# Performance work log

Hardware: AMD Instinct MI355X
Metric: run time of the kernel (lower is better)

Reference implementation:

```python
import jax, jax.numpy as jnp
import numpy as np

L = 1000  # fixed waveform length implied by MaxPool1d(1000) and [:, :, :1000] slices


def _conv1d(x, w, pad, reflect=False):
    # x: [B, Cin, T], w: [Cout, Cin, K]; torch conv1d == cross-correlation == lax conv
    if reflect:
        x = jnp.pad(x, ((0, 0), (0, 0), (pad, pad)), mode='reflect')
        pads = [(0, 0)]
    else:
        pads = [(pad, pad)]
    return jax.lax.conv_general_dilated(x, w, (1,), pads,
                                        dimension_numbers=('NCH', 'OIH', 'NCH'))


def setup_inputs() -> dict:
    key = jax.random.key(0)
    ks = jax.random.split(key, 10)
    B = 4096
    s = 0.1  # weight init scale
    return {
        'wf': jax.random.normal(ks[0], (B, 1, L), jnp.float32),
        'mask': jnp.ones((B, L), jnp.float32),
        'SPE': jax.random.uniform(ks[1], (L,), jnp.float32),
        'w_cum_area': jax.random.normal(ks[2], (1, 1, 121), jnp.float32) * s,
        'w_x': jax.random.normal(ks[3], (1, 1, 121), jnp.float32) * s,
        'w_div': jax.random.normal(ks[4], (1, 1, 121), jnp.float32) * s,
        'w_roll': jax.random.normal(ks[5], (1, 1, 101), jnp.float32) * s,
        'w_sub': jax.random.normal(ks[6], (15, 3, 21), jnp.float32) * s,
        'w_comb': jax.random.normal(ks[7], (1, 1, 5, 101, 3), jnp.float32) * s,
        'W_param': jnp.array([0.0, 5.0, 10.0], jnp.float32),
    }


def reference(wf, mask, SPE, w_cum_area, w_x, w_div, w_roll, w_sub, w_comb, W_param):
    B = wf.shape[0]
    # fixed (non-learned) derivative + running-mean kernels from __init__
    div_x_w = jnp.array([1/280, -4/105, 1/5, -4/5, 0.0, 4/5, -1/5, 4/105, -1/280],
                        jnp.float32).reshape(1, 1, 9)
    run_mean_w = jnp.full((1, 1, 51), 1.0 / 51, jnp.float32)

    # h = MaxPool1d(1000)(wf).squeeze(1).tile(1,3) / SPE.amax(); tiling == broadcast
    h = wf.max(axis=(1, 2))[:, None] / SPE.max()            # [B,1]
    W = jax.nn.softmax(-jax.nn.relu(h - W_param), axis=1)   # [B,3]

    cum_area = jnp.cumsum(wf, axis=-1)                      # [B,1,L]
    div_x_smd = _conv1d(_conv1d(wf, div_x_w, 4), run_mean_w, 25)  # zero-padded convs

    BL = _conv1d(cum_area, w_roll, 100, reflect=True)[:, :, :L] * w_cum_area.sum()
    fit_cum = jax.nn.relu(_conv1d(cum_area, w_cum_area, 100, reflect=True)[:, :, :L] - BL)
    fit_x = jax.nn.relu(_conv1d(wf, w_x, 100, reflect=True))[:, :, :L]
    fit_div = jax.nn.relu(_conv1d(div_x_smd, w_div, 100, reflect=True))[:, :, :L]

    features1 = jnp.concatenate([fit_cum, fit_x, fit_div], axis=1)   # [B,3,L]
    S = features1.sum(axis=2, keepdims=True) + 1e-10
    features1_norm = features1 / S

    features2 = _conv1d(features1_norm, w_sub, 10, reflect=True)     # [B,15,L]
    # [B,L,15] -> [B,L,5,3], weight the 3-way split by per-sample W
    fc = features2.transpose(0, 2, 1).reshape(B, L, 5, 3) * W[:, None, None, :]
    fc = fc.transpose(0, 2, 1, 3)[:, None]                           # [B,1,5,L,3]

    out = jax.lax.conv_general_dilated(fc, w_comb, (1, 1, 1),
                                       [(0, 0), (50, 50), (0, 0)],
                                       dimension_numbers=('NCDHW', 'OIDHW', 'NCDHW'))
    out = jax.nn.softplus(out).reshape(B, L)                         # [B,L]

    amax = out.max(axis=1, keepdims=True) + 1e-10
    out_norm = out / amax * mask
    return jax.nn.softmax(1e4 * out_norm, axis=1)
```

## Files before the change

kernel.cpp:

```cpp
#include <hip/hip_runtime.h>
#include <math.h>

#define TPB 256
#define LW  1000
#define CSTR 1124

#define OFF_WFE   0
#define OFF_CUME  1200
#define OFF_DSE   2400
#define OFF_F1E   3600
#define OFF_D1    3600
#define OFF_SCAND 4600
#define OFF_OUTB  6972
#define OFF_RED   7972
#define SMEM_F    7980
#define OFF_KC    0
#define OFF_WS2   384
#define OFF_F2V   1344

__device__ __forceinline__ float4 ld4(const float* p) { return *(const float4*)p; }

__device__ __forceinline__ float blk_red_max(float v, float* red) {
  #pragma unroll
  for (int o = 32; o > 0; o >>= 1) v = fmaxf(v, __shfl_xor(v, o, 64));
  const int w = threadIdx.x >> 6;
  if ((threadIdx.x & 63) == 0) red[w] = v;
  __syncthreads();
  float r = fmaxf(fmaxf(red[0], red[1]), fmaxf(red[2], red[3]));
  __syncthreads();
  return r;
}

__device__ __forceinline__ float blk_red_sum(float v, float* red) {
  #pragma unroll
  for (int o = 32; o > 0; o >>= 1) v += __shfl_xor(v, o, 64);
  const int w = threadIdx.x >> 6;
  if ((threadIdx.x & 63) == 0) red[w] = v;
  __syncthreads();
  float r = red[0] + red[1] + red[2] + red[3];
  __syncthreads();
  return r;
}

__device__ __forceinline__ int refl(int j) {
  return j < 0 ? -j : (j >= LW ? 2 * LW - 2 - j : j);
}

extern "C" __global__ void prep_kernel(const float* __restrict__ wsub_g,
                                       const float* __restrict__ wcb_g,
                                       float* __restrict__ P) {
  const int task = blockIdx.x * blockDim.x + threadIdx.x;
  if (task >= 1089) return;
  const int m = task / 363;
  const int r = task - m * 363;
  const int cin = r / 121;
  const int k = r - cin * 121;
  float acc = 0.f;
  for (int q = 0; q < 5; ++q) {
    const int ch = 3 * q + m;
    const float* ws = wsub_g + (ch * 3 + cin) * 21;
    #pragma unroll
    for (int j = 0; j < 21; ++j) {
      const int a = k - j;
      if (a >= 0 && a <= 100) acc = fmaf(ws[j], wcb_g[q * 303 + a * 3 + m], acc);
    }
  }
  P[task] = acc;
}

extern "C" __global__ void __launch_bounds__(TPB, 5)
spot_kernel(const float* __restrict__ wf_g,  const float* __restrict__ mask_g,
            const float* __restrict__ spe_g, const float* __restrict__ wca_g,
            const float* __restrict__ wx_g,  const float* __restrict__ wdv_g,
            const float* __restrict__ wrl_g, const float* __restrict__ wsub_g,
            const float* __restrict__ wcb_g, const float* __restrict__ wp_g,
            const float* __restrict__ P_g,   float* __restrict__ out_g)
{
  __shared__ __align__(16) float sm[SMEM_F];
  const int tid = threadIdx.x;
  const int b = blockIdx.x;
  const float* wf = wf_g + (size_t)b * LW;
  float* red = sm + OFF_RED;

  float hmx = -INFINITY;
  for (int i = tid; i < 1200; i += TPB) sm[OFF_WFE + i] = wf[refl(i - 100)];
  for (int t = tid; t < LW; t += TPB) hmx = fmaxf(hmx, wf[t]);
  float smx = -INFINITY;
  for (int t = tid; t < LW; t += TPB) smx = fmaxf(smx, spe_g[t]);
  double* scand = (double*)(sm + OFF_SCAND);
  double l0 = 0, l1 = 0, l2 = 0, l3 = 0;
  if (tid < 250) {
    l0 = (double)wf[4 * tid + 0];
    l1 = l0 + (double)wf[4 * tid + 1];
    l2 = l1 + (double)wf[4 * tid + 2];
    l3 = l2 + (double)wf[4 * tid + 3];
  }
  scand[tid] = l3;

  hmx = blk_red_max(hmx, red);
  smx = blk_red_max(smx, red);

  const float h = hmx / smx;
  float a0 = -fmaxf(h - wp_g[0], 0.f);
  float a1 = -fmaxf(h - wp_g[1], 0.f);
  float a2 = -fmaxf(h - wp_g[2], 0.f);
  float am = fmaxf(a0, fmaxf(a1, a2));
  float e0 = expf(a0 - am), e1 = expf(a1 - am), e2 = expf(a2 - am);
  float es = e0 + e1 + e2;
  float Wv[3] = { e0 / es, e1 / es, e2 / es };
  float swca = 0.f;
  for (int k = 0; k < 121; ++k) swca += wca_g[k];

  if (tid < 64) {
    double s0 = scand[4 * tid], s1 = scand[4 * tid + 1];
    double s2 = scand[4 * tid + 2], s3 = scand[4 * tid + 3];
    double tot = s0 + s1 + s2 + s3;
    double inc = tot;
    #pragma unroll
    for (int o = 1; o < 64; o <<= 1) {
      double n = __shfl_up(inc, o, 64);
      if ((tid & 63) >= o) inc += n;
    }
    double ex = inc - tot;
    scand[4 * tid]     = ex;
    scand[4 * tid + 1] = ex + s0;
    scand[4 * tid + 2] = ex + s0 + s1;
    scand[4 * tid + 3] = ex + s0 + s1 + s2;
  }
  __syncthreads();
  if (tid < 250) {
    double base = scand[tid];
    float4 cv = { (float)(base + l0), (float)(base + l1),
                  (float)(base + l2), (float)(base + l3) };
    *(float4*)(sm + OFF_CUME + 100 + 4 * tid) = cv;
  }
  const float dker[9] = {1.f/280.f, -4.f/105.f, 0.2f, -0.8f, 0.f, 0.8f, -0.2f, 4.f/105.f, -1.f/280.f};
  for (int t = tid; t < LW; t += TPB) {
    float a = 0.f;
    #pragma unroll
    for (int k = 0; k < 9; ++k) {
      if (k == 4) continue;
      int j = t + k - 4;
      float x = (j >= 0 && j < LW) ? sm[OFF_WFE + 100 + j] : 0.f;
      a = fmaf(dker[k], x, a);
    }
    sm[OFF_D1 + t] = a;
  }
  __syncthreads();
  for (int i = tid; i < 100; i += TPB) {
    sm[OFF_CUME + i]        = sm[OFF_CUME + 200 - i];
    sm[OFF_CUME + 1100 + i] = sm[OFF_CUME + 1098 - i];
  }
  for (int t = tid; t < LW; t += TPB) {
    int lo = t - 25 < 0 ? 0 : t - 25;
    int hi = t + 25 >= LW ? LW - 1 : t + 25;
    float a = 0.f;
    for (int j = lo; j <= hi; ++j) a += sm[OFF_D1 + j];
    sm[OFF_DSE + 100 + t] = a * (1.f / 51.f);
  }
  __syncthreads();
  for (int i = tid; i < 100; i += TPB) {
    sm[OFF_DSE + i]        = sm[OFF_DSE + 200 - i];
    sm[OFF_DSE + 1100 + i] = sm[OFF_DSE + 1098 - i];
  }
  __syncthreads();

  float lsC = 0.f, lsX = 0.f, lsD = 0.f;
  if (tid < 250) {
    const int t0 = 4 * tid;
    const float* ce = sm + OFF_CUME + t0;
    const float* we = sm + OFF_WFE + t0;
    const float* de = sm + OFF_DSE + t0;
    float cw_[8], ww_[8], dw_[8];
    *(float4*)cw_ = ld4(ce); *(float4*)(cw_ + 4) = ld4(ce + 4);
    *(float4*)ww_ = ld4(we); *(float4*)(ww_ + 4) = ld4(we + 4);
    *(float4*)dw_ = ld4(de); *(float4*)(dw_ + 4) = ld4(de + 4);
    float aC[4] = {0,0,0,0}, aB[4] = {0,0,0,0}, aX[4] = {0,0,0,0}, aD[4] = {0,0,0,0};
    for (int g = 0; g < 120; g += 4) {
      #pragma unroll
      for (int kk = 0; kk < 4; ++kk) {
        const int k = g + kk;
        const float wa = wca_g[k], wxk = wx_g[k], wdk = wdv_g[k];
        #pragma unroll
        for (int j = 0; j < 4; ++j) {
          aC[j] = fmaf(wa,  cw_[kk + j], aC[j]);
          aX[j] = fmaf(wxk, ww_[kk + j], aX[j]);
          aD[j] = fmaf(wdk, dw_[kk + j], aD[j]);
        }
        if (k <= 100) {
          const float wr = wrl_g[k];
          #pragma unroll
          for (int j = 0; j < 4; ++j) aB[j] = fmaf(wr, cw_[kk + j], aB[j]);
        }
      }
      #pragma unroll
      for (int j = 0; j < 4; ++j) { cw_[j] = cw_[j+4]; ww_[j] = ww_[j+4]; dw_[j] = dw_[j+4]; }
      *(float4*)(cw_ + 4) = ld4(ce + g + 8);
      *(float4*)(ww_ + 4) = ld4(we + g + 8);
      *(float4*)(dw_ + 4) = ld4(de + g + 8);
    }
    {
      const float wa = wca_g[120], wxk = wx_g[120], wdk = wdv_g[120];
      #pragma unroll
      for (int j = 0; j < 4; ++j) {
        aC[j] = fmaf(wa,  cw_[j], aC[j]);
        aX[j] = fmaf(wxk, ww_[j], aX[j]);
        aD[j] = fmaf(wdk, dw_[j], aD[j]);
      }
    }
    float4 vC, vX, vD;
    float* pC = (float*)&vC; float* pX = (float*)&vX; float* pD = (float*)&vD;
    #pragma unroll
    for (int j = 0; j < 4; ++j) {
      float fc = fmaxf(fmaf(-aB[j], swca, aC[j]), 0.f);
      float fx = fmaxf(aX[j], 0.f);
      float fd = fmaxf(aD[j], 0.f);
      pC[j] = fc; pX[j] = fx; pD[j] = fd;
      lsC += fc; lsX += fx; lsD += fd;
    }
    *(float4*)(sm + OFF_F1E + 0 * CSTR + 60 + t0) = vC;
    *(float4*)(sm + OFF_F1E + 1 * CSTR + 60 + t0) = vX;
    *(float4*)(sm + OFF_F1E + 2 * CSTR + 60 + t0) = vD;
  }
  const float SC = blk_red_sum(lsC, red) + 1e-10f;
  const float SX = blk_red_sum(lsX, red) + 1e-10f;
  const float SD = blk_red_sum(lsD, red) + 1e-10f;
  {
    const float iC = 1.f / SC, iX = 1.f / SX, iD = 1.f / SD;
    for (int t = tid; t < LW; t += TPB) {
      sm[OFF_F1E + 0 * CSTR + 60 + t] *= iC;
      sm[OFF_F1E + 1 * CSTR + 60 + t] *= iX;
      sm[OFF_F1E + 2 * CSTR + 60 + t] *= iD;
    }
  }
  __syncthreads();

  for (int i = tid; i < 372; i += TPB) {
    const int c = i / 124, j = i - c * 124;
    const int dst = (j < 60) ? j : (1000 + j);
    const int src = (j < 60) ? (120 - j) : (1118 - j);
    sm[OFF_F1E + c * CSTR + dst] = sm[OFF_F1E + c * CSTR + src];
  }
  for (int i = tid; i < 363; i += TPB) {
    const int cin = i / 121, k = i - cin * 121;
    const float* Pp = P_g + cin * 121 + k;
    sm[OFF_KC + cin * 124 + k] =
        fmaf(Wv[0], Pp[0], fmaf(Wv[1], Pp[363], Wv[2] * Pp[726]));
  }
  for (int i = tid; i < 945; i += TPB) sm[OFF_WS2 + i] = wsub_g[i];
  __syncthreads();

  if (tid < 250) {
    const int t0 = 4 * tid;
    float acc[4] = {0,0,0,0};
    #pragma unroll
    for (int cin = 0; cin < 3; ++cin) {
      const float* xr = sm + OFF_F1E + cin * CSTR + t0;
      const float* kc = sm + OFF_KC + cin * 124;
      float xw[8];
      *(float4*)xw = ld4(xr); *(float4*)(xw + 4) = ld4(xr + 4);
      for (int g = 0; g < 120; g += 4) {
        #pragma unroll
        for (int kk = 0; kk < 4; ++kk) {
          const float w = kc[g + kk];
          #pragma unroll
          for (int j = 0; j < 4; ++j) acc[j] = fmaf(w, xw[kk + j], acc[j]);
        }
        #pragma unroll
        for (int j = 0; j < 4; ++j) xw[j] = xw[j + 4];
        *(float4*)(xw + 4) = ld4(xr + g + 8);
      }
      const float w120 = kc[120];
      #pragma unroll
      for (int j = 0; j < 4; ++j) acc[j] = fmaf(w120, xw[j], acc[j]);
    }
    float4 st = {acc[0], acc[1], acc[2], acc[3]};
    *(float4*)(sm + OFF_OUTB + t0) = st;
  }
  for (int task = tid; task < 1500; task += TPB) {
    const int ch = task / 100, up = task - ch * 100;
    const int u = (up < 50) ? (up - 50) : (950 + up);
    float acc2 = 0.f;
    #pragma unroll
    for (int cin = 0; cin < 3; ++cin) {
      const float* xr = sm + OFF_F1E + cin * CSTR + (50 + u);
      const float* wr = sm + OFF_WS2 + (ch * 3 + cin) * 21;
      #pragma unroll
      for (int j = 0; j < 21; ++j) acc2 = fmaf(wr[j], xr[j], acc2);
    }
    sm[OFF_F2V + ch * 100 + up] = acc2;
  }
  __syncthreads();

  if (tid < 100) {
    float corr = 0.f;
    if (tid < 50) {
      const int t = tid;
      for (int a = 0; a < 50; ++a) {
        if (t + a <= 49) {
          const int up = t + a;
          #pragma unroll
          for (int m = 0; m < 3; ++m) {
            const float wvm = Wv[m];
            #pragma unroll
            for (int q = 0; q < 5; ++q)
              corr = fmaf(wvm * wcb_g[q * 303 + a * 3 + m],
                          sm[OFF_F2V + (3 * q + m) * 100 + up], corr);
          }
        }
      }
      sm[OFF_OUTB + t] -= corr;
    } else {
      const int tp = tid;
      const int t = 900 + tp;
      for (int d = 0; d < 50; ++d) {
        if (tp - d >= 50) {
          const int up = tp - d;
          const int a = 100 - d;
          #pragma unroll
          for (int m = 0; m < 3; ++m) {
            const float wvm = Wv[m];
            #pragma unroll
            for (int q = 0; q < 5; ++q)
              corr = fmaf(wvm * wcb_g[q * 303 + a * 3 + m],
                          sm[OFF_F2V + (3 * q + m) * 100 + up], corr);
          }
        }
      }
      sm[OFF_OUTB + t] -= corr;
    }
  }
  __syncthreads();

  float lm = -INFINITY;
  for (int t = tid; t < LW; t += TPB) {
    float z = sm[OFF_OUTB + t];
    float sp = fmaxf(z, 0.f) + log1pf(expf(-fabsf(z)));
    sm[OFF_OUTB + t] = sp;
    lm = fmaxf(lm, sp);
  }
  const float amax = blk_red_max(lm, red) + 1e-10f;
  const float* mrow = mask_g + (size_t)b * LW;
  float lm2 = -INFINITY;
  for (int t = tid; t < LW; t += TPB) {
    float v = 1e4f * (sm[OFF_OUTB + t] / amax) * mrow[t];
    sm[OFF_OUTB + t] = v;
    lm2 = fmaxf(lm2, v);
  }
  const float m2 = blk_red_max(lm2, red);
  float ls = 0.f;
  for (int t = tid; t < LW; t += TPB) {
    float e = expf(sm[OFF_OUTB + t] - m2);
    sm[OFF_OUTB + t] = e;
    ls += e;
  }
  const float S2 = blk_red_sum(ls, red);
  const float invs = 1.f / S2;
  float* orow = out_g + (size_t)b * LW;
  for (int t = tid; t < LW; t += TPB) orow[t] = sm[OFF_OUTB + t] * invs;
}

extern "C" void kernel_launch(void* const* d_in, const int* in_sizes, int n_in,
                              void* d_out, int out_size, void* d_ws, size_t ws_size,
                              hipStream_t stream) {
  (void)n_in; (void)ws_size; (void)out_size;
  const float* wf   = (const float*)d_in[0];
  const float* mask = (const float*)d_in[1];
  const float* spe  = (const float*)d_in[2];
  const float* wca  = (const float*)d_in[3];
  const float* wx   = (const float*)d_in[4];
  const float* wdv  = (const float*)d_in[5];
  const float* wrl  = (const float*)d_in[6];
  const float* wsub = (const float*)d_in[7];
  const float* wcb  = (const float*)d_in[8];
  const float* wp   = (const float*)d_in[9];
  float* P = (float*)d_ws;
  const int B = in_sizes[0] / LW;
  hipLaunchKernelGGL(prep_kernel, dim3(5), dim3(TPB), 0, stream, wsub, wcb, P);
  hipLaunchKernelGGL(spot_kernel, dim3(B), dim3(TPB), 0, stream,
                     wf, mask, spe, wca, wx, wdv, wrl, wsub, wcb, wp, P, (float*)d_out);
}
```

Baseline: 338.2 us.

## Use prefix-sum running mean, hoist SPE max and weight sum, keep outputs in registers

The 51-tap running mean is now computed as a difference of a prefix sum of the derivative signal. The SPE max and the w_cum_area sum move into the prep kernel, and the wf loads are vectorised. The edge-correction convolution is restructured into vectorised blocked tasks. The final softplus/softmax stages keep each thread's four outputs in registers instead of a shared buffer, which shrinks shared memory and allows raising launch bounds from 5 to 6 blocks. A float prefix sum may lose some precision compared with the direct 51-term sum.

```diff
diff --git a/kernel.cpp b/kernel.cpp
--- a/kernel.cpp
+++ b/kernel.cpp
@@ -6,17 +6,17 @@
 #define CSTR 1124
 
 #define OFF_WFE   0
-#define OFF_CUME  1200
-#define OFF_DSE   2400
-#define OFF_F1E   3600
-#define OFF_D1    3600
-#define OFF_SCAND 4600
-#define OFF_OUTB  6972
-#define OFF_RED   7972
-#define SMEM_F    7980
+#define OFF_CUME  1120
+#define OFF_DSE   2240
+#define OFF_F1E   3360
+#define OFF_SCAND 3360
+#define OFF_C     3872
+#define OFF_RED   6740
+#define SMEM_F    6748
 #define OFF_KC    0
-#define OFF_WS2   384
-#define OFF_F2V   1344
+#define OFF_WS2   376
+#define OFF_F2V   1456
+#define OFF_PART  0
 
 __device__ __forceinline__ float4 ld4(const float* p) { return *(const float4*)p; }
 
@@ -46,29 +46,71 @@
   return j < 0 ? -j : (j >= LW ? 2 * LW - 2 - j : j);
 }
 
+template<int OFF0>
+__device__ __forceinline__ void f2v_accum(const float* xr, const float* wr, float acc[4]) {
+  float xw[12];
+  *(float4*)xw       = ld4(xr);
+  *(float4*)(xw + 4) = ld4(xr + 4);
+  *(float4*)(xw + 8) = ld4(xr + 8);
+  #pragma unroll
+  for (int jb = 0; jb < 20; jb += 4) {
+    float4 w4 = ld4(wr + jb);
+    const float wv[4] = {w4.x, w4.y, w4.z, w4.w};
+    #pragma unroll
+    for (int kk = 0; kk < 4; ++kk)
+      #pragma unroll
+      for (int o = 0; o < 4; ++o)
+        acc[o] = fmaf(wv[kk], xw[OFF0 + kk + o], acc[o]);
+    #pragma unroll
+    for (int j = 0; j < 8; ++j) xw[j] = xw[j + 4];
+    *(float4*)(xw + 8) = ld4(xr + jb + 12);
+  }
+  const float w20 = wr[20];
+  #pragma unroll
+  for (int o = 0; o < 4; ++o) acc[o] = fmaf(w20, xw[OFF0 + o], acc[o]);
+}
+
 extern "C" __global__ void prep_kernel(const float* __restrict__ wsub_g,
                                        const float* __restrict__ wcb_g,
+                                       const float* __restrict__ wca_g,
+                                       const float* __restrict__ spe_g,
                                        float* __restrict__ P) {
+  __shared__ float sred[4];
   const int task = blockIdx.x * blockDim.x + threadIdx.x;
-  if (task >= 1089) return;
-  const int m = task / 363;
-  const int r = task - m * 363;
-  const int cin = r / 121;
-  const int k = r - cin * 121;
-  float acc = 0.f;
-  for (int q = 0; q < 5; ++q) {
-    const int ch = 3 * q + m;
-    const float* ws = wsub_g + (ch * 3 + cin) * 21;
-    #pragma unroll
-    for (int j = 0; j < 21; ++j) {
-      const int a = k - j;
-      if (a >= 0 && a <= 100) acc = fmaf(ws[j], wcb_g[q * 303 + a * 3 + m], acc);
-    }
-  }
-  P[task] = acc;
-}
-
-extern "C" __global__ void __launch_bounds__(TPB, 5)
+  if (task < 1089) {
+    const int m = task / 363;
+    const int r = task - m * 363;
+    const int cin = r / 121;
+    const int k = r - cin * 121;
+    float acc = 0.f;
+    for (int q = 0; q < 5; ++q) {
+      const int ch = 3 * q + m;
+      const float* ws = wsub_g + (ch * 3 + cin) * 21;
+      #pragma unroll
+      for (int j = 0; j < 21; ++j) {
+        const int a = k - j;
+        if (a >= 0 && a <= 100) acc = fmaf(ws[j], wcb_g[q * 303 + a * 3 + m], acc);
+      }
+    }
+    P[task] = acc;
+  } else if (task == 1089) {
+    float s = 0.f;
+    for (int k = 0; k < 121; ++k) s += wca_g[k];
+    P[1089] = s;
+  }
+  if (blockIdx.x == 4) {
+    float mx = -INFINITY;
+    for (int t = threadIdx.x; t < LW; t += TPB) mx = fmaxf(mx, spe_g[t]);
+    #pragma unroll
+    for (int o = 32; o > 0; o >>= 1) mx = fmaxf(mx, __shfl_xor(mx, o, 64));
+    if ((threadIdx.x & 63) == 0) sred[threadIdx.x >> 6] = mx;
+    __syncthreads();
+    if (threadIdx.x == 0)
+      P[1090] = fmaxf(fmaxf(sred[0], sred[1]), fmaxf(sred[2], sred[3]));
+  }
+}
+
+extern "C" __global__ void __launch_bounds__(TPB, 6)
 spot_kernel(const float* __restrict__ wf_g,  const float* __restrict__ mask_g,
             const float* __restrict__ spe_g, const float* __restrict__ wca_g,
             const float* __restrict__ wx_g,  const float* __restrict__ wdv_g,
@@ -81,25 +123,25 @@
   const int b = blockIdx.x;
   const float* wf = wf_g + (size_t)b * LW;
   float* red = sm + OFF_RED;
-
-  float hmx = -INFINITY;
-  for (int i = tid; i < 1200; i += TPB) sm[OFF_WFE + i] = wf[refl(i - 100)];
-  for (int t = tid; t < LW; t += TPB) hmx = fmaxf(hmx, wf[t]);
-  float smx = -INFINITY;
-  for (int t = tid; t < LW; t += TPB) smx = fmaxf(smx, spe_g[t]);
+  const int t0 = 4 * tid;
+
+  for (int i = tid; i < 1120; i += TPB) sm[OFF_WFE + i] = wf[refl(i - 100)];
   double* scand = (double*)(sm + OFF_SCAND);
   double l0 = 0, l1 = 0, l2 = 0, l3 = 0;
-  if (tid < 250) {
-    l0 = (double)wf[4 * tid + 0];
-    l1 = l0 + (double)wf[4 * tid + 1];
-    l2 = l1 + (double)wf[4 * tid + 2];
-    l3 = l2 + (double)wf[4 * tid + 3];
+  float hmx = -INFINITY;
+  if (tid < 250) {
+    float4 wv4 = ld4(wf + t0);
+    hmx = fmaxf(fmaxf(wv4.x, wv4.y), fmaxf(wv4.z, wv4.w));
+    l0 = (double)wv4.x;
+    l1 = l0 + (double)wv4.y;
+    l2 = l1 + (double)wv4.z;
+    l3 = l2 + (double)wv4.w;
   }
   scand[tid] = l3;
-
   hmx = blk_red_max(hmx, red);
-  smx = blk_red_max(smx, red);
-
+
+  const float smx = P_g[1090];
+  const float swca = P_g[1089];
   const float h = hmx / smx;
   float a0 = -fmaxf(h - wp_g[0], 0.f);
   float a1 = -fmaxf(h - wp_g[1], 0.f);
@@ -108,8 +150,6 @@
   float e0 = expf(a0 - am), e1 = expf(a1 - am), e2 = expf(a2 - am);
   float es = e0 + e1 + e2;
   float Wv[3] = { e0 / es, e1 / es, e2 / es };
-  float swca = 0.f;
-  for (int k = 0; k < 121; ++k) swca += wca_g[k];
 
   if (tid < 64) {
     double s0 = scand[4 * tid], s1 = scand[4 * tid + 1];
@@ -132,42 +172,79 @@
     double base = scand[tid];
     float4 cv = { (float)(base + l0), (float)(base + l1),
                   (float)(base + l2), (float)(base + l3) };
-    *(float4*)(sm + OFF_CUME + 100 + 4 * tid) = cv;
+    *(float4*)(sm + OFF_CUME + 100 + t0) = cv;
   }
   const float dker[9] = {1.f/280.f, -4.f/105.f, 0.2f, -0.8f, 0.f, 0.8f, -0.2f, 4.f/105.f, -1.f/280.f};
+  float dv0 = 0, dv1 = 0, dv2 = 0, dv3 = 0;
+  if (tid >= 1 && tid <= 248) {
+    float xw[12];
+    const float* xr = sm + OFF_WFE + t0 + 96;
+    *(float4*)xw = ld4(xr); *(float4*)(xw+4) = ld4(xr+4); *(float4*)(xw+8) = ld4(xr+8);
+    float d[4];
+    #pragma unroll
+    for (int j = 0; j < 4; ++j) {
+      float a = 0.f;
+      #pragma unroll
+      for (int k = 0; k < 9; ++k) {
+        if (k == 4) continue;
+        a = fmaf(dker[k], xw[j + k], a);
+      }
+      d[j] = a;
+    }
+    dv0 = d[0]; dv1 = d[1]; dv2 = d[2]; dv3 = d[3];
+  } else if (tid == 0 || tid == 249) {
+    float d[4];
+    #pragma unroll
+    for (int j = 0; j < 4; ++j) {
+      float a = 0.f;
+      for (int k = 0; k < 9; ++k) {
+        if (k == 4) continue;
+        const int o = t0 + j - 4 + k;
+        if (o >= 0 && o < LW) a = fmaf(dker[k], sm[OFF_WFE + 100 + o], a);
+      }
+      d[j] = a;
+    }
+    dv0 = d[0]; dv1 = d[1]; dv2 = d[2]; dv3 = d[3];
+  }
+  {
+    const float s0 = dv0, s1 = s0 + dv1, s2 = s1 + dv2, s3 = s2 + dv3;
+    float inc = s3;
+    const int lane = tid & 63;
+    #pragma unroll
+    for (int o = 1; o < 64; o <<= 1) {
+      float n = __shfl_up(inc, o, 64);
+      if (lane >= o) inc += n;
+    }
+    float* redw = red + 4;
+    if (lane == 63) redw[tid >> 6] = inc;
+    __syncthreads();
+    float base = 0.f;
+    for (int w = 0; w < (tid >> 6); ++w) base += redw[w];
+    if (tid < 250) {
+      const float ex = base + inc - s3;
+      float4 cv = { ex + s0, ex + s1, ex + s2, ex + s3 };
+      *(float4*)(sm + OFF_C + t0) = cv;
+    }
+  }
+  __syncthreads();
   for (int t = tid; t < LW; t += TPB) {
-    float a = 0.f;
-    #pragma unroll
-    for (int k = 0; k < 9; ++k) {
-      if (k == 4) continue;
-      int j = t + k - 4;
-      float x = (j >= 0 && j < LW) ? sm[OFF_WFE + 100 + j] : 0.f;
-      a = fmaf(dker[k], x, a);
-    }
-    sm[OFF_D1 + t] = a;
-  }
-  __syncthreads();
-  for (int i = tid; i < 100; i += TPB) {
-    sm[OFF_CUME + i]        = sm[OFF_CUME + 200 - i];
-    sm[OFF_CUME + 1100 + i] = sm[OFF_CUME + 1098 - i];
-  }
-  for (int t = tid; t < LW; t += TPB) {
-    int lo = t - 25 < 0 ? 0 : t - 25;
-    int hi = t + 25 >= LW ? LW - 1 : t + 25;
-    float a = 0.f;
-    for (int j = lo; j <= hi; ++j) a += sm[OFF_D1 + j];
-    sm[OFF_DSE + 100 + t] = a * (1.f / 51.f);
-  }
-  __syncthreads();
-  for (int i = tid; i < 100; i += TPB) {
-    sm[OFF_DSE + i]        = sm[OFF_DSE + 200 - i];
-    sm[OFF_DSE + 1100 + i] = sm[OFF_DSE + 1098 - i];
+    const float hi = sm[OFF_C + (t + 25 > 999 ? 999 : t + 25)];
+    const float lo = (t >= 26) ? sm[OFF_C + t - 26] : 0.f;
+    sm[OFF_DSE + 100 + t] = (hi - lo) * (1.f / 51.f);
+  }
+  for (int i = tid; i < 120; i += TPB) {
+    if (i < 100) sm[OFF_CUME + i] = sm[OFF_CUME + 200 - i];
+    else         sm[OFF_CUME + 1000 + i] = sm[OFF_CUME + 2198 - (1000 + i)];
+  }
+  __syncthreads();
+  for (int i = tid; i < 120; i += TPB) {
+    if (i < 100) sm[OFF_DSE + i] = sm[OFF_DSE + 200 - i];
+    else         sm[OFF_DSE + 1000 + i] = sm[OFF_DSE + 2198 - (1000 + i)];
   }
   __syncthreads();
 
   float lsC = 0.f, lsX = 0.f, lsD = 0.f;
   if (tid < 250) {
-    const int t0 = 4 * tid;
     const float* ce = sm + OFF_CUME + t0;
     const float* we = sm + OFF_WFE + t0;
     const float* de = sm + OFF_DSE + t0;
@@ -176,7 +253,31 @@
     *(float4*)ww_ = ld4(we); *(float4*)(ww_ + 4) = ld4(we + 4);
     *(float4*)dw_ = ld4(de); *(float4*)(dw_ + 4) = ld4(de + 4);
     float aC[4] = {0,0,0,0}, aB[4] = {0,0,0,0}, aX[4] = {0,0,0,0}, aD[4] = {0,0,0,0};
-    for (int g = 0; g < 120; g += 4) {
+    for (int g = 0; g < 100; g += 4) {
+      #pragma unroll
+      for (int kk = 0; kk < 4; ++kk) {
+        const int k = g + kk;
+        const float wa = wca_g[k], wxk = wx_g[k], wdk = wdv_g[k], wr = wrl_g[k];
+        #pragma unroll
+        for (int j = 0; j < 4; ++j) {
+          aC[j] = fmaf(wa,  cw_[kk + j], aC[j]);
+          aB[j] = fmaf(wr,  cw_[kk + j], aB[j]);
+          aX[j] = fmaf(wxk, ww_[kk + j], aX[j]);
+          aD[j] = fmaf(wdk, dw_[kk + j], aD[j]);
+        }
+      }
+      #pragma unroll
+      for (int j = 0; j < 4; ++j) { cw_[j] = cw_[j+4]; ww_[j] = ww_[j+4]; dw_[j] = dw_[j+4]; }
+      *(float4*)(cw_ + 4) = ld4(ce + g + 8);
+      *(float4*)(ww_ + 4) = ld4(we + g + 8);
+      *(float4*)(dw_ + 4) = ld4(de + g + 8);
+    }
+    {
+      const float wr100 = wrl_g[100];
+      #pragma unroll
+      for (int j = 0; j < 4; ++j) aB[j] = fmaf(wr100, cw_[j], aB[j]);
+    }
+    for (int g = 100; g < 116; g += 4) {
       #pragma unroll
       for (int kk = 0; kk < 4; ++kk) {
         const int k = g + kk;
@@ -187,11 +288,6 @@
           aX[j] = fmaf(wxk, ww_[kk + j], aX[j]);
           aD[j] = fmaf(wdk, dw_[kk + j], aD[j]);
         }
-        if (k <= 100) {
-          const float wr = wrl_g[k];
-          #pragma unroll
-          for (int j = 0; j < 4; ++j) aB[j] = fmaf(wr, cw_[kk + j], aB[j]);
-        }
       }
       #pragma unroll
       for (int j = 0; j < 4; ++j) { cw_[j] = cw_[j+4]; ww_[j] = ww_[j+4]; dw_[j] = dw_[j+4]; }
@@ -199,13 +295,15 @@
       *(float4*)(ww_ + 4) = ld4(we + g + 8);
       *(float4*)(dw_ + 4) = ld4(de + g + 8);
     }
-    {
-      const float wa = wca_g[120], wxk = wx_g[120], wdk = wdv_g[120];
+    #pragma unroll
+    for (int kk = 0; kk < 5; ++kk) {
+      const int k = 116 + kk;
+      const float wa = wca_g[k], wxk = wx_g[k], wdk = wdv_g[k];
       #pragma unroll
       for (int j = 0; j < 4; ++j) {
-        aC[j] = fmaf(wa,  cw_[j], aC[j]);
-        aX[j] = fmaf(wxk, ww_[j], aX[j]);
-        aD[j] = fmaf(wdk, dw_[j], aD[j]);
+        aC[j] = fmaf(wa,  cw_[kk + j], aC[j]);
+        aX[j] = fmaf(wxk, ww_[kk + j], aX[j]);
+        aD[j] = fmaf(wdk, dw_[kk + j], aD[j]);
       }
     }
     float4 vC, vX, vD;
@@ -235,8 +333,8 @@
   }
   __syncthreads();
 
-  for (int i = tid; i < 372; i += TPB) {
-    const int c = i / 124, j = i - c * 124;
+  for (int i = tid; i < 360; i += TPB) {
+    const int c = i / 120, j = i - c * 120;
     const int dst = (j < 60) ? j : (1000 + j);
     const int src = (j < 60) ? (120 - j) : (1118 - j);
     sm[OFF_F1E + c * CSTR + dst] = sm[OFF_F1E + c * CSTR + src];
@@ -247,12 +345,14 @@
     sm[OFF_KC + cin * 124 + k] =
         fmaf(Wv[0], Pp[0], fmaf(Wv[1], Pp[363], Wv[2] * Pp[726]));
   }
-  for (int i = tid; i < 945; i += TPB) sm[OFF_WS2 + i] = wsub_g[i];
-  __syncthreads();
-
-  if (tid < 250) {
-    const int t0 = 4 * tid;
-    float acc[4] = {0,0,0,0};
+  for (int i = tid; i < 1080; i += TPB) {
+    const int row = i / 24, k = i - row * 24;
+    sm[OFF_WS2 + i] = (k < 21) ? wsub_g[row * 21 + k] : 0.f;
+  }
+  __syncthreads();
+
+  float res[4] = {0, 0, 0, 0};
+  if (tid < 250) {
     #pragma unroll
     for (int cin = 0; cin < 3; ++cin) {
       const float* xr = sm + OFF_F1E + cin * CSTR + t0;
@@ -260,104 +360,135 @@
       float xw[8];
       *(float4*)xw = ld4(xr); *(float4*)(xw + 4) = ld4(xr + 4);
       for (int g = 0; g < 120; g += 4) {
+        float4 kw = ld4(kc + g);
+        const float wv[4] = {kw.x, kw.y, kw.z, kw.w};
         #pragma unroll
-        for (int kk = 0; kk < 4; ++kk) {
-          const float w = kc[g + kk];
+        for (int kk = 0; kk < 4; ++kk)
           #pragma unroll
-          for (int j = 0; j < 4; ++j) acc[j] = fmaf(w, xw[kk + j], acc[j]);
-        }
+          for (int j = 0; j < 4; ++j) res[j] = fmaf(wv[kk], xw[kk + j], res[j]);
         #pragma unroll
         for (int j = 0; j < 4; ++j) xw[j] = xw[j + 4];
         *(float4*)(xw + 4) = ld4(xr + g + 8);
       }
       const float w120 = kc[120];
       #pragma unroll
-      for (int j = 0; j < 4; ++j) acc[j] = fmaf(w120, xw[j], acc[j]);
-    }
-    float4 st = {acc[0], acc[1], acc[2], acc[3]};
-    *(float4*)(sm + OFF_OUTB + t0) = st;
-  }
-  for (int task = tid; task < 1500; task += TPB) {
-    const int ch = task / 100, up = task - ch * 100;
-    const int u = (up < 50) ? (up - 50) : (950 + up);
-    float acc2 = 0.f;
-    #pragma unroll
-    for (int cin = 0; cin < 3; ++cin) {
-      const float* xr = sm + OFF_F1E + cin * CSTR + (50 + u);
-      const float* wr = sm + OFF_WS2 + (ch * 3 + cin) * 21;
-      #pragma unroll
-      for (int j = 0; j < 21; ++j) acc2 = fmaf(wr[j], xr[j], acc2);
-    }
-    sm[OFF_F2V + ch * 100 + up] = acc2;
-  }
-  __syncthreads();
-
-  if (tid < 100) {
-    float corr = 0.f;
-    if (tid < 50) {
-      const int t = tid;
-      for (int a = 0; a < 50; ++a) {
-        if (t + a <= 49) {
-          const int up = t + a;
-          #pragma unroll
-          for (int m = 0; m < 3; ++m) {
-            const float wvm = Wv[m];
-            #pragma unroll
-            for (int q = 0; q < 5; ++q)
-              corr = fmaf(wvm * wcb_g[q * 303 + a * 3 + m],
-                          sm[OFF_F2V + (3 * q + m) * 100 + up], corr);
-          }
-        }
-      }
-      sm[OFF_OUTB + t] -= corr;
+      for (int j = 0; j < 4; ++j) res[j] = fmaf(w120, xw[j], res[j]);
+    }
+  }
+  for (int task = tid; task < 390; task += TPB) {
+    const int side = (task >= 195) ? 1 : 0;
+    const int r = task - 195 * side;
+    const int ch = r / 13;
+    const int gl = r - 13 * ch;
+    float acc[4] = {0, 0, 0, 0};
+    const float* wrb = sm + OFF_WS2 + ch * 72;
+    if (side == 0) {
+      const int xb = 4 * gl;
+      #pragma unroll
+      for (int cin = 0; cin < 3; ++cin)
+        f2v_accum<0>(sm + OFF_F1E + cin * CSTR + xb, wrb + cin * 24, acc);
     } else {
-      const int tp = tid;
-      const int t = 900 + tp;
-      for (int d = 0; d < 50; ++d) {
-        if (tp - d >= 50) {
-          const int up = tp - d;
-          const int a = 100 - d;
-          #pragma unroll
-          for (int m = 0; m < 3; ++m) {
-            const float wvm = Wv[m];
-            #pragma unroll
-            for (int q = 0; q < 5; ++q)
-              corr = fmaf(wvm * wcb_g[q * 303 + a * 3 + m],
-                          sm[OFF_F2V + (3 * q + m) * 100 + up], corr);
-          }
-        }
-      }
-      sm[OFF_OUTB + t] -= corr;
-    }
-  }
-  __syncthreads();
-
+      const int xb = 1048 + 4 * gl;
+      #pragma unroll
+      for (int cin = 0; cin < 3; ++cin)
+        f2v_accum<2>(sm + OFF_F1E + cin * CSTR + xb, wrb + cin * 24, acc);
+    }
+    const int dst = OFF_F2V + ch * 104 + side * 52 + 4 * gl;
+    if (gl < 12) {
+      float4 st = {acc[0], acc[1], acc[2], acc[3]};
+      *(float4*)(sm + dst) = st;
+    } else {
+      sm[dst] = acc[0]; sm[dst + 1] = acc[1];
+    }
+  }
+  __syncthreads();
+
+  for (int task = tid; task < 500; task += TPB) {
+    const int q = task / 100;
+    const int tcol = task - q * 100;
+    const float* f0 = sm + OFF_F2V + (3 * q) * 104;
+    float acc = 0.f;
+    if (tcol < 50) {
+      const int t = tcol;
+      for (int a = 0; a <= 49 - t; ++a) {
+        const int up = t + a;
+        const float* wb = wcb_g + q * 303 + a * 3;
+        acc = fmaf(Wv[0] * wb[0], f0[up], acc);
+        acc = fmaf(Wv[1] * wb[1], f0[104 + up], acc);
+        acc = fmaf(Wv[2] * wb[2], f0[208 + up], acc);
+      }
+    } else {
+      const int tp = tcol;
+      for (int d = 0; d <= tp - 50; ++d) {
+        const int up = tp - d + 2;
+        const int a = 100 - d;
+        const float* wb = wcb_g + q * 303 + a * 3;
+        acc = fmaf(Wv[0] * wb[0], f0[up], acc);
+        acc = fmaf(Wv[1] * wb[1], f0[104 + up], acc);
+        acc = fmaf(Wv[2] * wb[2], f0[208 + up], acc);
+      }
+    }
+    sm[OFF_PART + task] = acc;
+  }
+  __syncthreads();
+
+  if (tid < 250 && (t0 < 52 || t0 >= 948)) {
+    #pragma unroll
+    for (int j = 0; j < 4; ++j) {
+      const int t = t0 + j;
+      if (t < 50) {
+        float c = 0.f;
+        #pragma unroll
+        for (int q = 0; q < 5; ++q) c += sm[OFF_PART + q * 100 + t];
+        res[j] -= c;
+      } else if (t >= 950) {
+        const int tc = t - 900;
+        float c = 0.f;
+        #pragma unroll
+        for (int q = 0; q < 5; ++q) c += sm[OFF_PART + q * 100 + tc];
+        res[j] -= c;
+      }
+    }
+  }
+  float sp[4];
   float lm = -INFINITY;
-  for (int t = tid; t < LW; t += TPB) {
-    float z = sm[OFF_OUTB + t];
-    float sp = fmaxf(z, 0.f) + log1pf(expf(-fabsf(z)));
-    sm[OFF_OUTB + t] = sp;
-    lm = fmaxf(lm, sp);
+  if (tid < 250) {
+    #pragma unroll
+    for (int j = 0; j < 4; ++j) {
+      const float z = res[j];
+      sp[j] = fmaxf(z, 0.f) + log1pf(expf(-fabsf(z)));
+      lm = fmaxf(lm, sp[j]);
+    }
   }
   const float amax = blk_red_max(lm, red) + 1e-10f;
-  const float* mrow = mask_g + (size_t)b * LW;
+  float v4[4];
   float lm2 = -INFINITY;
-  for (int t = tid; t < LW; t += TPB) {
-    float v = 1e4f * (sm[OFF_OUTB + t] / amax) * mrow[t];
-    sm[OFF_OUTB + t] = v;
-    lm2 = fmaxf(lm2, v);
+  if (tid < 250) {
+    const float4 mv = ld4(mask_g + (size_t)b * LW + t0);
+    const float* mj = (const float*)&mv;
+    const float ia = 1e4f / amax;
+    #pragma unroll
+    for (int j = 0; j < 4; ++j) {
+      v4[j] = (sp[j] * ia) * mj[j];
+      lm2 = fmaxf(lm2, v4[j]);
+    }
   }
   const float m2 = blk_red_max(lm2, red);
   float ls = 0.f;
-  for (int t = tid; t < LW; t += TPB) {
-    float e = expf(sm[OFF_OUTB + t] - m2);
-    sm[OFF_OUTB + t] = e;
-    ls += e;
+  float e4[4];
+  if (tid < 250) {
+    #pragma unroll
+    for (int j = 0; j < 4; ++j) {
+      e4[j] = expf(v4[j] - m2);
+      ls += e4[j];
+    }
   }
   const float S2 = blk_red_sum(ls, red);
-  const float invs = 1.f / S2;
-  float* orow = out_g + (size_t)b * LW;
-  for (int t = tid; t < LW; t += TPB) orow[t] = sm[OFF_OUTB + t] * invs;
+  if (tid < 250) {
+    const float invs = 1.f / S2;
+    float4 st = { e4[0] * invs, e4[1] * invs, e4[2] * invs, e4[3] * invs };
+    *(float4*)(out_g + (size_t)b * LW + t0) = st;
+  }
 }
 
 extern "C" void kernel_launch(void* const* d_in, const int* in_sizes, int n_in,
@@ -376,7 +507,7 @@
   const float* wp   = (const float*)d_in[9];
   float* P = (float*)d_ws;
   const int B = in_sizes[0] / LW;
-  hipLaunchKernelGGL(prep_kernel, dim3(5), dim3(TPB), 0, stream, wsub, wcb, P);
+  hipLaunchKernelGGL(prep_kernel, dim3(5), dim3(TPB), 0, stream, wsub, wcb, wca, spe, P);
   hipLaunchKernelGGL(spot_kernel, dim3(B), dim3(TPB), 0, stream,
                      wf, mask, spe, wca, wx, wdv, wrl, wsub, wcb, wp, P, (float*)d_out);
 }
```

New measurement: 283.2 us. 1.19x faster.
